# Kernel tuning notes

Hardware: AMD Instinct MI355X
Metric: run time of the kernel (lower is better)

## Reference

```python
import jax, jax.numpy as jnp
import numpy as np

B, C, HC, H, W = 4, 512, 64, 64, 64


def _spectral_norm(Wm, u):
    # one torch-style power iteration; u,v are treated as constants (detached)
    v = Wm.T @ u
    v = v / jnp.maximum(jnp.linalg.norm(v), 1e-12)
    u2 = Wm @ v
    u2 = u2 / jnp.maximum(jnp.linalg.norm(u2), 1e-12)
    u2 = jax.lax.stop_gradient(u2)
    v = jax.lax.stop_gradient(v)
    sigma = u2 @ (Wm @ v)
    return Wm / sigma


def setup_inputs() -> dict:
    key = jax.random.key(0)
    ks = jax.random.split(key, 14)
    return {
        "x": jax.random.normal(ks[0], (B, C, H, W), jnp.float32),
        "Wf": jax.random.normal(ks[1], (HC, C), jnp.float32) * 0.05,
        "bf": jax.random.normal(ks[2], (HC,), jnp.float32) * 0.05,
        "Wg": jax.random.normal(ks[3], (HC, C), jnp.float32) * 0.05,
        "bg": jax.random.normal(ks[4], (HC,), jnp.float32) * 0.05,
        "Wh": jax.random.normal(ks[5], (HC, C), jnp.float32) * 0.05,
        "bh": jax.random.normal(ks[6], (HC,), jnp.float32) * 0.05,
        "Wv": jax.random.normal(ks[7], (C, HC), jnp.float32) * 0.05,
        "bv": jax.random.normal(ks[8], (C,), jnp.float32) * 0.05,
        "uf": jax.random.normal(ks[9], (HC,), jnp.float32),
        "ug": jax.random.normal(ks[10], (HC,), jnp.float32),
        "uh": jax.random.normal(ks[11], (HC,), jnp.float32),
        "uv": jax.random.normal(ks[12], (C,), jnp.float32),
        "gamma": jax.random.normal(ks[13], (1,), jnp.float32),
    }


def reference(x, Wf, bf, Wg, bg, Wh, bh, Wv, bv, uf, ug, uh, uv, gamma):
    nb, nc, imgh, imgw = x.shape
    n = imgh * imgw
    xf = x.reshape(nb, nc, n)  # [B, C, N]
    Wf_sn = _spectral_norm(Wf, uf)
    Wg_sn = _spectral_norm(Wg, ug)
    Wh_sn = _spectral_norm(Wh, uh)
    Wv_sn = _spectral_norm(Wv, uv)
    # 1x1 convs are per-pixel GEMMs
    f = jnp.einsum('kc,bcn->bkn', Wf_sn, xf) + bf[:, None]  # [B, HC, N]
    g = jnp.einsum('kc,bcn->bkn', Wg_sn, xf) + bg[:, None]
    h = jnp.einsum('kc,bcn->bkn', Wh_sn, xf) + bh[:, None]
    s = jnp.einsum('bkn,bkm->bnm', f, g)       # [B, N, N] scores
    beta = jax.nn.softmax(s, axis=-1)
    o = jnp.einsum('bnm,bkm->bkn', beta, h)    # [B, HC, N] (already transposed)
    out = jnp.einsum('ck,bkn->bcn', Wv_sn, o) + bv[:, None]
    out = out.reshape(nb, nc, imgh, imgw)
    return gamma[0] * out + x
```

## Files before the change

kernel.cpp:

```cpp
#include <hip/hip_runtime.h>
#include <hip/hip_bf16.h>

typedef __attribute__((ext_vector_type(8))) short short8;
typedef __attribute__((ext_vector_type(4))) float floatx4;
typedef __attribute__((ext_vector_type(16))) float floatx16;
typedef unsigned short ushortt;

#define LOG2E 1.4426950408889634f

__device__ __forceinline__ float fast_exp2(float x) {
    return __builtin_amdgcn_exp2f(x);
}
__device__ __forceinline__ ushortt f2bf(float f) {
    unsigned int u = __float_as_uint(f);
    u += 0x7fffu + ((u >> 16) & 1u);
    return (ushortt)(u >> 16);
}
__device__ __forceinline__ unsigned int f2bf_pk(float a, float b) {
    float2 t; t.x = a; t.y = b;
    __hip_bfloat162 h = __float22bfloat162_rn(t);
    return *reinterpret_cast<unsigned int*>(&h);
}
__device__ __forceinline__ float bf2f(ushortt h) {
    return __uint_as_float(((unsigned int)h) << 16);
}

__device__ __forceinline__ float block_sum(float v, float* red) {
    #pragma unroll
    for (int off = 32; off > 0; off >>= 1) v += __shfl_down(v, off);
    int wid = threadIdx.x >> 6, ln = threadIdx.x & 63;
    __syncthreads();
    if (ln == 0) red[wid] = v;
    __syncthreads();
    return red[0] + red[1] + red[2] + red[3];
}

__global__ __launch_bounds__(256) void sigma_kernel(
    const float* __restrict__ Wf, const float* __restrict__ uf,
    const float* __restrict__ Wg, const float* __restrict__ ug,
    const float* __restrict__ Wh, const float* __restrict__ uh,
    const float* __restrict__ Wv, const float* __restrict__ uv,
    float* __restrict__ sig,
    ushortt* __restrict__ wqkv, ushortt* __restrict__ wvb) {
    __shared__ float tv[512];
    __shared__ float tvp[256];
    __shared__ float zpart[256];
    __shared__ float red[4];
    __shared__ float ssig;
    const int mat = blockIdx.x, tid = threadIdx.x;

    if (mat < 3) {
        const float* W = (mat == 0) ? Wf : ((mat == 1) ? Wg : Wh);
        const float* u = (mat == 0) ? uf : ((mat == 1) ? ug : uh);
        for (int c = tid; c < 512; c += 256) {
            float s0 = 0.f;
            #pragma unroll 8
            for (int r = 0; r < 64; ++r) s0 += W[r * 512 + c] * u[r];
            tv[c] = s0;
        }
        __syncthreads();
        float p = tv[tid] * tv[tid] + tv[tid + 256] * tv[tid + 256];
        float nt2 = block_sum(p, red);
        float nt = fmaxf(sqrtf(nt2), 1e-12f);
        {
            int r = tid & 63, qq = tid >> 6;
            const float* Wr = W + r * 512 + qq * 128;
            const float* tq = tv + qq * 128;
            float part = 0.f;
            #pragma unroll 16
            for (int c = 0; c < 128; ++c) part += Wr[c] * tq[c];
            zpart[tid] = part;
        }
        __syncthreads();
        if (tid < 64) {
            float z = zpart[tid] + zpart[tid + 64] + zpart[tid + 128] + zpart[tid + 192];
            z = z * z;
            #pragma unroll
            for (int off = 32; off > 0; off >>= 1) z += __shfl_xor(z, off);
            if (tid == 0) {
                float sg0 = sqrtf(z) / nt;
                sig[mat] = sg0;
                ssig = sg0;
            }
        }
        __syncthreads();
        float inv = 1.0f / ssig;
        const float4* W4 = reinterpret_cast<const float4*>(W);
        unsigned int* dst = reinterpret_cast<unsigned int*>(wqkv + mat * 32768);
        for (int i = tid; i < 8192; i += 256) {
            float4 wv = W4[i];
            dst[2 * i]     = f2bf_pk(wv.x * inv, wv.y * inv);
            dst[2 * i + 1] = f2bf_pk(wv.z * inv, wv.w * inv);
        }
    } else {
        const float* W = Wv; const float* u = uv;
        {
            int c = tid & 63, rs = tid >> 6;
            float s0 = 0.f;
            #pragma unroll 8
            for (int r = rs * 128; r < rs * 128 + 128; ++r) s0 += W[r * 64 + c] * u[r];
            tvp[tid] = s0;
        }
        __syncthreads();
        if (tid < 64) tv[tid] = tvp[tid] + tvp[tid + 64] + tvp[tid + 128] + tvp[tid + 192];
        __syncthreads();
        float t = (tid < 64) ? tv[tid] : 0.f;
        float nt2 = block_sum(t * t, red);
        float nt = fmaxf(sqrtf(nt2), 1e-12f);
        float sg3;
        {
            const float* w1 = W + (size_t)tid * 64;
            const float* w2 = W + (size_t)(tid + 256) * 64;
            float z1 = 0.f, z2 = 0.f;
            #pragma unroll 8
            for (int c = 0; c < 64; ++c) {
                float tc = tv[c];
                z1 += w1[c] * tc;
                z2 += w2[c] * tc;
            }
            float zp = z1 * z1 + z2 * z2;
            float z2t = block_sum(zp, red);
            sg3 = sqrtf(z2t) / nt;
            if (tid == 0) sig[3] = sg3;
        }
        float inv = 1.0f / sg3;
        const float4* W4 = reinterpret_cast<const float4*>(W);
        unsigned int* dst = reinterpret_cast<unsigned int*>(wvb);
        for (int i = tid; i < 8192; i += 256) {
            float4 wv = W4[i];
            dst[2 * i]     = f2bf_pk(wv.x * inv, wv.y * inv);
            dst[2 * i + 1] = f2bf_pk(wv.z * inv, wv.w * inv);
        }
    }
}

__global__ __launch_bounds__(256, 4) void qkv_kernel(
    const float* __restrict__ x, const ushortt* __restrict__ wqkv,
    const float* __restrict__ bfv, const float* __restrict__ bgv,
    const float* __restrict__ bhv,
    ushortt* __restrict__ Qb, ushortt* __restrict__ Kb, ushortt* __restrict__ Vt) {
    __shared__ unsigned int xs[2048];
    const int tid = threadIdx.x;
    const int n0 = blockIdx.x * 32, b = blockIdx.y;
    const int lane = tid & 63, w = tid >> 6;
    const int strip = w & 1, ksel = w >> 1;
    const int q = lane >> 4, l15 = lane & 15;
    const int sn = tid & 31, sg = tid >> 5;

    floatx4 acc[6];
    #pragma unroll
    for (int kt = 0; kt < 6; ++kt) acc[kt] = (floatx4){0.f, 0.f, 0.f, 0.f};

    const float* xb = x + ((size_t)b * 512) * 4096 + n0 + sn;
    const int sslot = sn * 32 + ((sg ^ (sn & 7)) << 2);
    float2 pre[4];
    #pragma unroll
    for (int i = 0; i < 4; ++i) {
        int c = sg * 8 + 2 * i;
        pre[i].x = xb[(size_t)c * 4096];
        pre[i].y = xb[(size_t)(c + 1) * 4096];
    }
    {
        uint4 pk;
        pk.x = f2bf_pk(pre[0].x, pre[0].y);
        pk.y = f2bf_pk(pre[1].x, pre[1].y);
        pk.z = f2bf_pk(pre[2].x, pre[2].y);
        pk.w = f2bf_pk(pre[3].x, pre[3].y);
        *reinterpret_cast<uint4*>(&xs[sslot]) = pk;
    }
    #pragma unroll
    for (int i = 0; i < 4; ++i) {
        int c = 64 + sg * 8 + 2 * i;
        pre[i].x = xb[(size_t)c * 4096];
        pre[i].y = xb[(size_t)(c + 1) * 4096];
    }

    for (int it = 0; it < 8; ++it) {
        __syncthreads();
        if (it < 7) {
            uint4 pk;
            pk.x = f2bf_pk(pre[0].x, pre[0].y);
            pk.y = f2bf_pk(pre[1].x, pre[1].y);
            pk.z = f2bf_pk(pre[2].x, pre[2].y);
            pk.w = f2bf_pk(pre[3].x, pre[3].y);
            *reinterpret_cast<uint4*>(&xs[(((it + 1) & 1) << 10) + sslot]) = pk;
        }
        if (it < 6) {
            #pragma unroll
            for (int i = 0; i < 4; ++i) {
                int c = (it + 2) * 64 + sg * 8 + 2 * i;
                pre[i].x = xb[(size_t)c * 4096];
                pre[i].y = xb[(size_t)(c + 1) * 4096];
            }
        }
        const int c0 = it * 64;
        const unsigned int* xr = &xs[((it & 1) << 10) + (16 * strip + l15) * 32];
        #pragma unroll
        for (int kc = 0; kc < 2; ++kc) {
            union { uint4 v; short8 s8; } af;
            af.v = *reinterpret_cast<const uint4*>(&xr[((4 * kc + q) ^ (l15 & 7)) << 2]);
            #pragma unroll
            for (int kt = 0; kt < 6; ++kt) {
                short8 bb = *reinterpret_cast<const short8*>(
                    &wqkv[(size_t)(ksel * 96 + kt * 16 + l15) * 512 + c0 + kc * 32 + q * 8]);
                acc[kt] = __builtin_amdgcn_mfma_f32_16x16x32_bf16(af.s8, bb, acc[kt], 0, 0, 0);
            }
        }
    }

    const int nloc = n0 + 16 * strip + 4 * q;
    if (ksel == 0) {
        #pragma unroll
        for (int kt = 0; kt < 4; ++kt) {
            int k = kt * 16 + l15;
            float bb = bfv[k];
            #pragma unroll
            for (int r = 0; r < 4; ++r)
                Qb[((size_t)b * 4096 + nloc + r) * 64 + k] = f2bf((acc[kt][r] + bb) * LOG2E);
        }
        #pragma unroll
        for (int kt = 4; kt < 6; ++kt) {
            int k = (kt - 4) * 16 + l15;
            float bb = bgv[k];
            #pragma unroll
            for (int r = 0; r < 4; ++r)
                Kb[((size_t)b * 4096 + nloc + r) * 64 + k] = f2bf(acc[kt][r] + bb);
        }
    } else {
        #pragma unroll
        for (int kt = 0; kt < 2; ++kt) {
            int k = 32 + kt * 16 + l15;
            float bb = bgv[k];
            #pragma unroll
            for (int r = 0; r < 4; ++r)
                Kb[((size_t)b * 4096 + nloc + r) * 64 + k] = f2bf(acc[kt][r] + bb);
        }
    }
    __syncthreads();
    if (ksel == 1) {
        #pragma unroll
        for (int kt = 2; kt < 6; ++kt) {
            int d = (kt - 2) * 16 + l15;
            float bb = bhv[d];
            int base = d * 17 + 8 * strip + 2 * q;
            xs[base]     = f2bf_pk(acc[kt][0] + bb, acc[kt][1] + bb);
            xs[base + 1] = f2bf_pk(acc[kt][2] + bb, acc[kt][3] + bb);
        }
    }
    __syncthreads();
    {
        int d = tid >> 2, sgg = tid & 3;
        uint4 vv;
        vv.x = xs[d * 17 + sgg * 4 + 0]; vv.y = xs[d * 17 + sgg * 4 + 1];
        vv.z = xs[d * 17 + sgg * 4 + 2]; vv.w = xs[d * 17 + sgg * 4 + 3];
        *reinterpret_cast<uint4*>(&Vt[((size_t)b * 64 + d) * 4096 + n0 + sgg * 8]) = vv;
    }
}

__global__ __launch_bounds__(256, 3) void attn_kernel(
    const ushortt* __restrict__ Qb, const ushortt* __restrict__ Kb,
    const ushortt* __restrict__ Vt, ushortt* __restrict__ Opart,
    float2* __restrict__ ml, ushortt* __restrict__ Ob, int KB) {
    __shared__ unsigned int smem[8448];
    const int tid = threadIdx.x;
    const int n0 = blockIdx.x * 64, b = blockIdx.y, s = blockIdx.z;
    const int lane = tid & 63, w = tid >> 6;
    const int qh = w & 1, kh = w >> 1;
    const int l31 = lane & 31, h = lane >> 5;

    const ushortt* Kg = Kb + (size_t)b * 4096 * 64;
    const ushortt* Vg = Vt + (size_t)b * 64 * 4096;

    short8 bq[4];
    {
        const ushortt* Qg = Qb + ((size_t)b * 4096 + n0 + 32 * qh + l31) * 64;
        #pragma unroll
        for (int kc = 0; kc < 4; ++kc)
            bq[kc] = *reinterpret_cast<const short8*>(Qg + kc * 16 + 8 * h);
    }

    floatx16 ot0 = {}, ot1 = {};
    float m_i = -1e30f, l_i = 0.f;

    const int row = tid >> 2, seg = tid & 3;
    const int kbeg = s * KB, kend = kbeg + KB;
    const int rsw = row & 7;
    const int ws0 = row * 32 + ((((2 * seg)) ^ rsw) << 2);
    const int ws1 = row * 32 + ((((2 * seg + 1)) ^ rsw) << 2);

    uint4 ck0, ck1, cv0, cv1;
    {
        int nb = kbeg * 64;
        const ushortt* kp = Kg + (size_t)(nb + row) * 64 + seg * 16;
        ck0 = *reinterpret_cast<const uint4*>(kp);
        ck1 = *reinterpret_cast<const uint4*>(kp + 8);
        const ushortt* vp = Vg + (size_t)row * 4096 + nb + seg * 16;
        cv0 = *reinterpret_cast<const uint4*>(vp);
        cv1 = *reinterpret_cast<const uint4*>(vp + 8);
    }
    *reinterpret_cast<uint4*>(&smem[ws0]) = ck0;
    *reinterpret_cast<uint4*>(&smem[ws1]) = ck1;
    *reinterpret_cast<uint4*>(&smem[2048 + ws0]) = cv0;
    *reinterpret_cast<uint4*>(&smem[2048 + ws1]) = cv1;
    if (kbeg + 1 < kend) {
        int nb = (kbeg + 1) * 64;
        const ushortt* kp = Kg + (size_t)(nb + row) * 64 + seg * 16;
        ck0 = *reinterpret_cast<const uint4*>(kp);
        ck1 = *reinterpret_cast<const uint4*>(kp + 8);
        const ushortt* vp = Vg + (size_t)row * 4096 + nb + seg * 16;
        cv0 = *reinterpret_cast<const uint4*>(vp);
        cv1 = *reinterpret_cast<const uint4*>(vp + 8);
    }

    for (int kb = kbeg; kb < kend; ++kb) {
        const int cur = (kb - kbeg) & 1;
        const unsigned int rb = cur ? 4096u : 0u;
        const unsigned int wbs = cur ? 0u : 4096u;
        __syncthreads();
        if (kb + 1 < kend) {
            *reinterpret_cast<uint4*>(&smem[wbs + ws0]) = ck0;
            *reinterpret_cast<uint4*>(&smem[wbs + ws1]) = ck1;
            *reinterpret_cast<uint4*>(&smem[wbs + 2048 + ws0]) = cv0;
            *reinterpret_cast<uint4*>(&smem[wbs + 2048 + ws1]) = cv1;
        }
        if (kb + 2 < kend) {
            int nb = (kb + 2) * 64;
            const ushortt* kp = Kg + (size_t)(nb + row) * 64 + seg * 16;
            ck0 = *reinterpret_cast<const uint4*>(kp);
            ck1 = *reinterpret_cast<const uint4*>(kp + 8);
            const ushortt* vp = Vg + (size_t)row * 4096 + nb + seg * 16;
            cv0 = *reinterpret_cast<const uint4*>(vp);
            cv1 = *reinterpret_cast<const uint4*>(vp + 8);
        }

        floatx16 st = {};
        const unsigned int* kr = &smem[rb + (32 * kh + l31) * 32];
        const int esw = l31 & 7;
        #pragma unroll
        for (int kc = 0; kc < 4; ++kc) {
            union { uint4 v; short8 s8; } af;
            af.v = *reinterpret_cast<const uint4*>(&kr[((2 * kc + h) ^ esw) << 2]);
            st = __builtin_amdgcn_mfma_f32_32x32x16_bf16(af.s8, bq[kc], st, 0, 0, 0);
        }

        float mx = fmaxf(fmaxf(fmaxf(st[0], st[1]), fmaxf(st[2], st[3])),
                         fmaxf(fmaxf(st[4], st[5]), fmaxf(st[6], st[7])));
        float mx2 = fmaxf(fmaxf(fmaxf(st[8], st[9]), fmaxf(st[10], st[11])),
                          fmaxf(fmaxf(st[12], st[13]), fmaxf(st[14], st[15])));
        mx = fmaxf(mx, mx2);
        mx = fmaxf(mx, __shfl_xor(mx, 32));
        if (!__all(mx <= m_i + 8.f)) {
            float mn = fmaxf(m_i, mx);
            float alpha = fast_exp2(m_i - mn);
            m_i = mn;
            l_i *= alpha;
            #pragma unroll
            for (int r = 0; r < 16; ++r) { ot0[r] *= alpha; ot1[r] *= alpha; }
        }
        float p[16], rs = 0.f;
        #pragma unroll
        for (int r = 0; r < 16; ++r) { p[r] = fast_exp2(st[r] - m_i); rs += p[r]; }
        rs += __shfl_xor(rs, 32);
        l_i += rs;

        unsigned int pk[8], sp[8];
        #pragma unroll
        for (int i = 0; i < 8; ++i) pk[i] = f2bf_pk(p[2 * i], p[2 * i + 1]);
        #pragma unroll
        for (int i = 0; i < 8; ++i) sp[i] = (unsigned int)__shfl_xor((int)pk[i], 32);
        union { unsigned int u[4]; short8 s8; } pb0, pb1;
        pb0.u[0] = h ? sp[2] : pk[0]; pb0.u[1] = h ? sp[3] : pk[1];
        pb0.u[2] = h ? pk[2] : sp[0]; pb0.u[3] = h ? pk[3] : sp[1];
        pb1.u[0] = h ? sp[6] : pk[4]; pb1.u[1] = h ? sp[7] : pk[5];
        pb1.u[2] = h ? pk[6] : sp[4]; pb1.u[3] = h ? pk[7] : sp[5];

        const unsigned int* vr0 = &smem[rb + 2048 + l31 * 32];
        const unsigned int* vr1 = &smem[rb + 2048 + (32 + l31) * 32];
        #pragma unroll
        for (int c = 0; c < 2; ++c) {
            union { uint4 v; short8 s8; } af;
            af.v = *reinterpret_cast<const uint4*>(&vr0[((4 * kh + 2 * c + h) ^ esw) << 2]);
            ot0 = __builtin_amdgcn_mfma_f32_32x32x16_bf16(af.s8, c ? pb1.s8 : pb0.s8, ot0, 0, 0, 0);
            af.v = *reinterpret_cast<const uint4*>(&vr1[((4 * kh + 2 * c + h) ^ esw) << 2]);
            ot1 = __builtin_amdgcn_mfma_f32_32x32x16_bf16(af.s8, c ? pb1.s8 : pb0.s8, ot1, 0, 0, 0);
        }
    }

    __syncthreads();
    if (h == 0) {
        smem[8192 + w * 32 + l31] = __float_as_uint(m_i);
        smem[8320 + w * 32 + l31] = __float_as_uint(l_i);
    }
    __syncthreads();
    int pw = 2 * (1 - kh) + qh;
    float m2 = __uint_as_float(smem[8192 + pw * 32 + l31]);
    float l2 = __uint_as_float(smem[8320 + pw * 32 + l31]);
    float mstar = fmaxf(m_i, m2);
    float wself = fast_exp2(m_i - mstar);
    float w2 = fast_exp2(m2 - mstar);
    float lm = wself * l_i + w2 * l2;
    float sc = (gridDim.z == 1) ? (wself / lm) : wself;
    if (gridDim.z > 1 && kh == 0 && h == 0) {
        float2 v; v.x = mstar; v.y = lm;
        ml[((size_t)s * 4 + b) * 4096 + n0 + 32 * qh + l31] = v;
    }
    float* om = reinterpret_cast<float*>(smem);
    if (kh == 0) {
        #pragma unroll
        for (int r = 0; r < 16; ++r) {
            int d0 = (r & 3) + 8 * (r >> 2) + 4 * h;
            om[(32 * qh + l31) * 65 + d0] = sc * ot0[r];
            om[(32 * qh + l31) * 65 + 32 + d0] = sc * ot1[r];
        }
    }
    __syncthreads();
    if (kh == 1) {
        #pragma unroll
        for (int r = 0; r < 16; ++r) {
            int d0 = (r & 3) + 8 * (r >> 2) + 4 * h;
            om[(32 * qh + l31) * 65 + d0] += sc * ot0[r];
            om[(32 * qh + l31) * 65 + 32 + d0] += sc * ot1[r];
        }
    }
    __syncthreads();
    {
        int qq = tid >> 2, dsg = tid & 3;
        unsigned int pkk[8];
        #pragma unroll
        for (int j = 0; j < 8; ++j)
            pkk[j] = f2bf_pk(om[qq * 65 + dsg * 16 + 2 * j], om[qq * 65 + dsg * 16 + 2 * j + 1]);
        ushortt* base = (gridDim.z == 1)
            ? (Ob + ((size_t)b * 4096 + n0) * 64)
            : (Opart + (((size_t)s * 4 + b) * 4096 + n0) * 64);
        uint4* d4 = reinterpret_cast<uint4*>(base + (size_t)qq * 64 + dsg * 16);
        uint4 o0; o0.x = pkk[0]; o0.y = pkk[1]; o0.z = pkk[2]; o0.w = pkk[3];
        uint4 o1; o1.x = pkk[4]; o1.y = pkk[5]; o1.z = pkk[6]; o1.w = pkk[7];
        d4[0] = o0; d4[1] = o1;
    }
}

__global__ __launch_bounds__(256, 2) void proj_kernel(
    const ushortt* __restrict__ Opart, const float2* __restrict__ ml,
    const ushortt* __restrict__ Ob, const ushortt* __restrict__ wvb,
    const float* __restrict__ bv, const float* __restrict__ gamma,
    const float* __restrict__ x, float* __restrict__ out, int S) {
    __shared__ ushortt ol[32 * 72];
    const int tid = threadIdx.x;
    const int n0 = blockIdx.x * 32, b = blockIdx.y;

    {
        int row = tid >> 3, t8 = tid & 7;
        int rg = n0 + row;
        if (S == 1) {
            uint4 v = *reinterpret_cast<const uint4*>(
                Ob + ((size_t)b * 4096 + rg) * 64 + t8 * 8);
            *reinterpret_cast<uint4*>(&ol[row * 72 + t8 * 8]) = v;
        } else {
            float2 mls[4];
            float m = -1e30f;
            #pragma unroll 4
            for (int s = 0; s < 4; ++s) {
                mls[s] = ml[((size_t)s * 4 + b) * 4096 + rg];
                m = fmaxf(m, mls[s].x);
            }
            float wgt[4], denom = 0.f;
            #pragma unroll 4
            for (int s = 0; s < 4; ++s) {
                wgt[s] = fast_exp2(mls[s].x - m);
                denom += wgt[s] * mls[s].y;
            }
            float inv = 1.0f / denom;
            float acc[8];
            #pragma unroll
            for (int j = 0; j < 8; ++j) acc[j] = 0.f;
            #pragma unroll 4
            for (int s = 0; s < 4; ++s) {
                union { uint4 v; ushortt hh[8]; } u;
                u.v = *reinterpret_cast<const uint4*>(
                    Opart + (((size_t)s * 4 + b) * 4096 + rg) * 64 + t8 * 8);
                float ww = wgt[s];
                #pragma unroll
                for (int j = 0; j < 8; ++j) acc[j] += ww * bf2f(u.hh[j]);
            }
            uint4 v;
            v.x = f2bf_pk(acc[0] * inv, acc[1] * inv);
            v.y = f2bf_pk(acc[2] * inv, acc[3] * inv);
            v.z = f2bf_pk(acc[4] * inv, acc[5] * inv);
            v.w = f2bf_pk(acc[6] * inv, acc[7] * inv);
            *reinterpret_cast<uint4*>(&ol[row * 72 + t8 * 8]) = v;
        }
    }
    __syncthreads();

    const int w = tid >> 6, lane = tid & 63, q = lane >> 4, l15 = lane & 15;
    short8 bfr[2][2];
    #pragma unroll
    for (int u = 0; u < 2; ++u)
        #pragma unroll
        for (int kc = 0; kc < 2; ++kc)
            bfr[u][kc] = *reinterpret_cast<const short8*>(
                &ol[(16 * u + l15) * 72 + 32 * kc + q * 8]);

    floatx4 acc[8][2];
    #pragma unroll
    for (int t = 0; t < 8; ++t)
        #pragma unroll
        for (int u = 0; u < 2; ++u) acc[t][u] = (floatx4){0.f, 0.f, 0.f, 0.f};

    const int cw = w * 128;
    #pragma unroll
    for (int t = 0; t < 8; ++t) {
        short8 a0 = *reinterpret_cast<const short8*>(
            &wvb[(size_t)(cw + 16 * t + l15) * 64 + q * 8]);
        short8 a1 = *reinterpret_cast<const short8*>(
            &wvb[(size_t)(cw + 16 * t + l15) * 64 + 32 + q * 8]);
        #pragma unroll
        for (int u = 0; u < 2; ++u) {
            acc[t][u] = __builtin_amdgcn_mfma_f32_16x16x32_bf16(a0, bfr[u][0], acc[t][u], 0, 0, 0);
            acc[t][u] = __builtin_amdgcn_mfma_f32_16x16x32_bf16(a1, bfr[u][1], acc[t][u], 0, 0, 0);
        }
    }

    float gm = gamma[0];
    #pragma unroll
    for (int t = 0; t < 8; ++t) {
        #pragma unroll
        for (int r = 0; r < 4; ++r) {
            int c = cw + 16 * t + 4 * q + r;
            float bb = bv[c];
            #pragma unroll
            for (int u = 0; u < 2; ++u) {
                int n = n0 + 16 * u + l15;
                size_t idx = ((size_t)(b * 512 + c)) * 4096 + n;
                out[idx] = gm * (acc[t][u][r] + bb) + x[idx];
            }
        }
    }
}

extern "C" void kernel_launch(void* const* d_in, const int* in_sizes, int n_in,
                              void* d_out, int out_size, void* d_ws, size_t ws_size,
                              hipStream_t stream) {
    const float* x   = (const float*)d_in[0];
    const float* Wf  = (const float*)d_in[1];
    const float* bf_ = (const float*)d_in[2];
    const float* Wg  = (const float*)d_in[3];
    const float* bg_ = (const float*)d_in[4];
    const float* Wh  = (const float*)d_in[5];
    const float* bh_ = (const float*)d_in[6];
    const float* Wv  = (const float*)d_in[7];
    const float* bv_ = (const float*)d_in[8];
    const float* uf  = (const float*)d_in[9];
    const float* ug  = (const float*)d_in[10];
    const float* uh  = (const float*)d_in[11];
    const float* uv  = (const float*)d_in[12];
    const float* gm  = (const float*)d_in[13];
    float* out = (float*)d_out;

    char* ws = (char*)d_ws;
    float*   sig   = (float*)ws;
    ushortt* wqkv  = (ushortt*)(ws + 256);
    ushortt* wvb   = (ushortt*)(ws + 196864);
    ushortt* Qb    = (ushortt*)(ws + 262400);
    ushortt* Kb    = (ushortt*)(ws + 2359552);
    ushortt* Vt    = (ushortt*)(ws + 4456704);
    ushortt* Ob    = (ushortt*)(ws + 6553856);
    float2*  ml    = (float2*)(ws + 8651008);
    ushortt* Opart = (ushortt*)(ws + 9175296);

    int S = (ws_size >= (size_t)17563904) ? 4 : 1;

    sigma_kernel<<<4, 256, 0, stream>>>(Wf, uf, Wg, ug, Wh, uh, Wv, uv, sig, wqkv, wvb);
    qkv_kernel<<<dim3(128, 4), 256, 0, stream>>>(x, wqkv, bf_, bg_, bh_, Qb, Kb, Vt);
    attn_kernel<<<dim3(64, 4, S), 256, 0, stream>>>(Qb, Kb, Vt, Opart, ml, Ob, 64 / S);
    proj_kernel<<<dim3(128, 4), 256, 0, stream>>>(Opart, ml, Ob, wvb, bv_, gm, x, out, S);
}
```

Measured before the change: 189.4 us.

## Fuse attention and output projection with per-wave key splits and XCD-aware mapping

Merges the attention and projection kernels into one. Each block now handles 32 queries, and each of its four waves processes a disjoint quarter of the keys using private double-buffered LDS tiles with no block barriers inside the loop. The partial softmax results are merged in LDS, then the Wv projection and residual add run in the same block. This removes the Opart/ml workspace round trip, the split-K grid dimension and one kernel launch. It adds XCD-aware block indexing so each batch maps to the same XCDs for L2 reuse, plus s_setprio around the MFMAs. In exchange, occupancy drops to 2 blocks per CU with larger LDS use, and each wave must load its own K/V tiles.

```diff
diff --git a/kernel.cpp b/kernel.cpp
--- a/kernel.cpp
+++ b/kernel.cpp
@@ -20,9 +20,6 @@
     float2 t; t.x = a; t.y = b;
     __hip_bfloat162 h = __float22bfloat162_rn(t);
     return *reinterpret_cast<unsigned int*>(&h);
-}
-__device__ __forceinline__ float bf2f(ushortt h) {
-    return __uint_as_float(((unsigned int)h) << 16);
 }
 
 __device__ __forceinline__ float block_sum(float v, float* red) {
@@ -257,15 +254,18 @@
     }
 }
 
-__global__ __launch_bounds__(256, 3) void attn_kernel(
+__global__ __launch_bounds__(256, 2) void attn_proj_kernel(
     const ushortt* __restrict__ Qb, const ushortt* __restrict__ Kb,
-    const ushortt* __restrict__ Vt, ushortt* __restrict__ Opart,
-    float2* __restrict__ ml, ushortt* __restrict__ Ob, int KB) {
-    __shared__ unsigned int smem[8448];
+    const ushortt* __restrict__ Vt, const ushortt* __restrict__ wvb,
+    const float* __restrict__ bv, const float* __restrict__ gamma,
+    const float* __restrict__ x, float* __restrict__ out) {
+    __shared__ unsigned int smem[16384];
     const int tid = threadIdx.x;
-    const int n0 = blockIdx.x * 64, b = blockIdx.y, s = blockIdx.z;
+    const int fid = blockIdx.x + 128 * blockIdx.y;
+    const int xcd = fid & 7, idx8 = fid >> 3;
+    const int b = xcd >> 1;
+    const int n0 = ((xcd & 1) * 64 + idx8) * 32;
     const int lane = tid & 63, w = tid >> 6;
-    const int qh = w & 1, kh = w >> 1;
     const int l31 = lane & 31, h = lane >> 5;
 
     const ushortt* Kg = Kb + (size_t)b * 4096 * 64;
@@ -273,7 +273,7 @@
 
     short8 bq[4];
     {
-        const ushortt* Qg = Qb + ((size_t)b * 4096 + n0 + 32 * qh + l31) * 64;
+        const ushortt* Qg = Qb + ((size_t)b * 4096 + n0 + l31) * 64;
         #pragma unroll
         for (int kc = 0; kc < 4; ++kc)
             bq[kc] = *reinterpret_cast<const short8*>(Qg + kc * 16 + 8 * h);
@@ -282,66 +282,57 @@
     floatx16 ot0 = {}, ot1 = {};
     float m_i = -1e30f, l_i = 0.f;
 
-    const int row = tid >> 2, seg = tid & 3;
-    const int kbeg = s * KB, kend = kbeg + KB;
-    const int rsw = row & 7;
-    const int ws0 = row * 32 + ((((2 * seg)) ^ rsw) << 2);
-    const int ws1 = row * 32 + ((((2 * seg + 1)) ^ rsw) << 2);
-
-    uint4 ck0, ck1, cv0, cv1;
-    {
-        int nb = kbeg * 64;
-        const ushortt* kp = Kg + (size_t)(nb + row) * 64 + seg * 16;
-        ck0 = *reinterpret_cast<const uint4*>(kp);
-        ck1 = *reinterpret_cast<const uint4*>(kp + 8);
-        const ushortt* vp = Vg + (size_t)row * 4096 + nb + seg * 16;
-        cv0 = *reinterpret_cast<const uint4*>(vp);
-        cv1 = *reinterpret_cast<const uint4*>(vp + 8);
-    }
-    *reinterpret_cast<uint4*>(&smem[ws0]) = ck0;
-    *reinterpret_cast<uint4*>(&smem[ws1]) = ck1;
-    *reinterpret_cast<uint4*>(&smem[2048 + ws0]) = cv0;
-    *reinterpret_cast<uint4*>(&smem[2048 + ws1]) = cv1;
-    if (kbeg + 1 < kend) {
-        int nb = (kbeg + 1) * 64;
-        const ushortt* kp = Kg + (size_t)(nb + row) * 64 + seg * 16;
-        ck0 = *reinterpret_cast<const uint4*>(kp);
-        ck1 = *reinterpret_cast<const uint4*>(kp + 8);
-        const ushortt* vp = Vg + (size_t)row * 4096 + nb + seg * 16;
-        cv0 = *reinterpret_cast<const uint4*>(vp);
-        cv1 = *reinterpret_cast<const uint4*>(vp + 8);
-    }
-
-    for (int kb = kbeg; kb < kend; ++kb) {
-        const int cur = (kb - kbeg) & 1;
-        const unsigned int rb = cur ? 4096u : 0u;
-        const unsigned int wbs = cur ? 0u : 4096u;
-        __syncthreads();
-        if (kb + 1 < kend) {
-            *reinterpret_cast<uint4*>(&smem[wbs + ws0]) = ck0;
-            *reinterpret_cast<uint4*>(&smem[wbs + ws1]) = ck1;
-            *reinterpret_cast<uint4*>(&smem[wbs + 2048 + ws0]) = cv0;
-            *reinterpret_cast<uint4*>(&smem[wbs + 2048 + ws1]) = cv1;
-        }
-        if (kb + 2 < kend) {
-            int nb = (kb + 2) * 64;
-            const ushortt* kp = Kg + (size_t)(nb + row) * 64 + seg * 16;
-            ck0 = *reinterpret_cast<const uint4*>(kp);
-            ck1 = *reinterpret_cast<const uint4*>(kp + 8);
-            const ushortt* vp = Vg + (size_t)row * 4096 + nb + seg * 16;
-            cv0 = *reinterpret_cast<const uint4*>(vp);
-            cv1 = *reinterpret_cast<const uint4*>(vp + 8);
-        }
+    const int krow = lane >> 3, kseg = lane & 7;
+    const int vsub = lane >> 2, vq = lane & 3;
+    const unsigned wb = (unsigned)w << 12;
+
+    uint4 ck[4], cv[4];
+    auto ldkv = [&](int t) {
+        const int pxb = t * 128 + 32 * w;
+        #pragma unroll
+        for (int p = 0; p < 4; ++p)
+            ck[p] = *reinterpret_cast<const uint4*>(
+                Kg + (size_t)(pxb + 8 * p + krow) * 64 + kseg * 8);
+        #pragma unroll
+        for (int p = 0; p < 4; ++p)
+            cv[p] = *reinterpret_cast<const uint4*>(
+                Vg + (size_t)(16 * p + vsub) * 4096 + pxb + vq * 8);
+    };
+    auto stkv = [&](int buf) {
+        const unsigned kb_ = wb + (buf ? 1024u : 0u);
+        const unsigned vb_ = wb + 2048u + (buf ? 1024u : 0u);
+        #pragma unroll
+        for (int p = 0; p < 4; ++p) {
+            int row = 8 * p + krow;
+            *reinterpret_cast<uint4*>(&smem[kb_ + row * 32 + ((kseg ^ (row & 7)) << 2)]) = ck[p];
+        }
+        #pragma unroll
+        for (int p = 0; p < 4; ++p) {
+            int d = 16 * p + vsub;
+            *reinterpret_cast<uint4*>(&smem[vb_ + d * 16 + ((vq ^ (d & 3)) << 2)]) = cv[p];
+        }
+    };
+
+    ldkv(0); stkv(0); ldkv(1);
+
+    for (int t = 0; t < 32; ++t) {
+        const int cur = t & 1;
+        if (t + 1 < 32) stkv(cur ^ 1);
+        if (t + 2 < 32) ldkv(t + 2);
 
         floatx16 st = {};
-        const unsigned int* kr = &smem[rb + (32 * kh + l31) * 32];
+        const unsigned kb_ = wb + (cur ? 1024u : 0u);
+        const unsigned vb_ = wb + 2048u + (cur ? 1024u : 0u);
         const int esw = l31 & 7;
+        const unsigned int* kr = &smem[kb_ + l31 * 32];
+        __builtin_amdgcn_s_setprio(1);
         #pragma unroll
         for (int kc = 0; kc < 4; ++kc) {
             union { uint4 v; short8 s8; } af;
             af.v = *reinterpret_cast<const uint4*>(&kr[((2 * kc + h) ^ esw) << 2]);
             st = __builtin_amdgcn_mfma_f32_32x32x16_bf16(af.s8, bq[kc], st, 0, 0, 0);
         }
+        __builtin_amdgcn_s_setprio(0);
 
         float mx = fmaxf(fmaxf(fmaxf(st[0], st[1]), fmaxf(st[2], st[3])),
                          fmaxf(fmaxf(st[4], st[5]), fmaxf(st[6], st[7])));
@@ -374,165 +365,115 @@
         pb1.u[0] = h ? sp[6] : pk[4]; pb1.u[1] = h ? sp[7] : pk[5];
         pb1.u[2] = h ? pk[6] : sp[4]; pb1.u[3] = h ? pk[7] : sp[5];
 
-        const unsigned int* vr0 = &smem[rb + 2048 + l31 * 32];
-        const unsigned int* vr1 = &smem[rb + 2048 + (32 + l31) * 32];
+        const unsigned int* vr0 = &smem[vb_ + l31 * 16];
+        const unsigned int* vr1 = &smem[vb_ + (32 + l31) * 16];
+        const int esv = l31 & 3;
+        __builtin_amdgcn_s_setprio(1);
         #pragma unroll
         for (int c = 0; c < 2; ++c) {
             union { uint4 v; short8 s8; } af;
-            af.v = *reinterpret_cast<const uint4*>(&vr0[((4 * kh + 2 * c + h) ^ esw) << 2]);
+            af.v = *reinterpret_cast<const uint4*>(&vr0[((2 * c + h) ^ esv) << 2]);
             ot0 = __builtin_amdgcn_mfma_f32_32x32x16_bf16(af.s8, c ? pb1.s8 : pb0.s8, ot0, 0, 0, 0);
-            af.v = *reinterpret_cast<const uint4*>(&vr1[((4 * kh + 2 * c + h) ^ esw) << 2]);
+            af.v = *reinterpret_cast<const uint4*>(&vr1[((2 * c + h) ^ esv) << 2]);
             ot1 = __builtin_amdgcn_mfma_f32_32x32x16_bf16(af.s8, c ? pb1.s8 : pb0.s8, ot1, 0, 0, 0);
         }
+        __builtin_amdgcn_s_setprio(0);
     }
 
     __syncthreads();
     if (h == 0) {
-        smem[8192 + w * 32 + l31] = __float_as_uint(m_i);
-        smem[8320 + w * 32 + l31] = __float_as_uint(l_i);
-    }
-    __syncthreads();
-    int pw = 2 * (1 - kh) + qh;
-    float m2 = __uint_as_float(smem[8192 + pw * 32 + l31]);
-    float l2 = __uint_as_float(smem[8320 + pw * 32 + l31]);
-    float mstar = fmaxf(m_i, m2);
-    float wself = fast_exp2(m_i - mstar);
-    float w2 = fast_exp2(m2 - mstar);
-    float lm = wself * l_i + w2 * l2;
-    float sc = (gridDim.z == 1) ? (wself / lm) : wself;
-    if (gridDim.z > 1 && kh == 0 && h == 0) {
-        float2 v; v.x = mstar; v.y = lm;
-        ml[((size_t)s * 4 + b) * 4096 + n0 + 32 * qh + l31] = v;
-    }
-    float* om = reinterpret_cast<float*>(smem);
-    if (kh == 0) {
-        #pragma unroll
-        for (int r = 0; r < 16; ++r) {
-            int d0 = (r & 3) + 8 * (r >> 2) + 4 * h;
-            om[(32 * qh + l31) * 65 + d0] = sc * ot0[r];
-            om[(32 * qh + l31) * 65 + 32 + d0] = sc * ot1[r];
-        }
-    }
-    __syncthreads();
-    if (kh == 1) {
-        #pragma unroll
-        for (int r = 0; r < 16; ++r) {
-            int d0 = (r & 3) + 8 * (r >> 2) + 4 * h;
-            om[(32 * qh + l31) * 65 + d0] += sc * ot0[r];
-            om[(32 * qh + l31) * 65 + 32 + d0] += sc * ot1[r];
-        }
+        smem[8704 + w * 32 + l31] = __float_as_uint(m_i);
+        smem[8832 + w * 32 + l31] = __float_as_uint(l_i);
     }
     __syncthreads();
     {
-        int qq = tid >> 2, dsg = tid & 3;
-        unsigned int pkk[8];
-        #pragma unroll
-        for (int j = 0; j < 8; ++j)
-            pkk[j] = f2bf_pk(om[qq * 65 + dsg * 16 + 2 * j], om[qq * 65 + dsg * 16 + 2 * j + 1]);
-        ushortt* base = (gridDim.z == 1)
-            ? (Ob + ((size_t)b * 4096 + n0) * 64)
-            : (Opart + (((size_t)s * 4 + b) * 4096 + n0) * 64);
-        uint4* d4 = reinterpret_cast<uint4*>(base + (size_t)qq * 64 + dsg * 16);
-        uint4 o0; o0.x = pkk[0]; o0.y = pkk[1]; o0.z = pkk[2]; o0.w = pkk[3];
-        uint4 o1; o1.x = pkk[4]; o1.y = pkk[5]; o1.z = pkk[6]; o1.w = pkk[7];
-        d4[0] = o0; d4[1] = o1;
-    }
-}
-
-__global__ __launch_bounds__(256, 2) void proj_kernel(
-    const ushortt* __restrict__ Opart, const float2* __restrict__ ml,
-    const ushortt* __restrict__ Ob, const ushortt* __restrict__ wvb,
-    const float* __restrict__ bv, const float* __restrict__ gamma,
-    const float* __restrict__ x, float* __restrict__ out, int S) {
-    __shared__ ushortt ol[32 * 72];
-    const int tid = threadIdx.x;
-    const int n0 = blockIdx.x * 32, b = blockIdx.y;
-
+        float mstar = -1e30f, mw[4], lw[4];
+        #pragma unroll
+        for (int w2 = 0; w2 < 4; ++w2) {
+            mw[w2] = __uint_as_float(smem[8704 + w2 * 32 + l31]);
+            lw[w2] = __uint_as_float(smem[8832 + w2 * 32 + l31]);
+            mstar = fmaxf(mstar, mw[w2]);
+        }
+        float lm = 0.f;
+        #pragma unroll
+        for (int w2 = 0; w2 < 4; ++w2) lm += fast_exp2(mw[w2] - mstar) * lw[w2];
+        float sc = fast_exp2(m_i - mstar) / lm;
+        float* reg = reinterpret_cast<float*>(&smem[w * 2176]);
+        #pragma unroll
+        for (int k = 0; k < 4; ++k) {
+            float4 v0, v1;
+            v0.x = sc * ot0[4 * k];     v0.y = sc * ot0[4 * k + 1];
+            v0.z = sc * ot0[4 * k + 2]; v0.w = sc * ot0[4 * k + 3];
+            v1.x = sc * ot1[4 * k];     v1.y = sc * ot1[4 * k + 1];
+            v1.z = sc * ot1[4 * k + 2]; v1.w = sc * ot1[4 * k + 3];
+            *reinterpret_cast<float4*>(&reg[l31 * 68 + 8 * k + 4 * h]) = v0;
+            *reinterpret_cast<float4*>(&reg[l31 * 68 + 32 + 8 * k + 4 * h]) = v1;
+        }
+    }
+    __syncthreads();
+    ushortt* ol = reinterpret_cast<ushortt*>(&smem[8960]);
     {
-        int row = tid >> 3, t8 = tid & 7;
-        int rg = n0 + row;
-        if (S == 1) {
-            uint4 v = *reinterpret_cast<const uint4*>(
-                Ob + ((size_t)b * 4096 + rg) * 64 + t8 * 8);
-            *reinterpret_cast<uint4*>(&ol[row * 72 + t8 * 8]) = v;
-        } else {
-            float2 mls[4];
-            float m = -1e30f;
-            #pragma unroll 4
-            for (int s = 0; s < 4; ++s) {
-                mls[s] = ml[((size_t)s * 4 + b) * 4096 + rg];
-                m = fmaxf(m, mls[s].x);
+        const int q = tid >> 3, d8 = (tid & 7) * 8;
+        float s[8];
+        #pragma unroll
+        for (int j = 0; j < 8; ++j) s[j] = 0.f;
+        #pragma unroll
+        for (int w2 = 0; w2 < 4; ++w2) {
+            const float* rr = reinterpret_cast<const float*>(&smem[w2 * 2176]) + q * 68 + d8;
+            float4 a = *reinterpret_cast<const float4*>(rr);
+            float4 b2 = *reinterpret_cast<const float4*>(rr + 4);
+            s[0] += a.x; s[1] += a.y; s[2] += a.z; s[3] += a.w;
+            s[4] += b2.x; s[5] += b2.y; s[6] += b2.z; s[7] += b2.w;
+        }
+        unsigned int* od = reinterpret_cast<unsigned int*>(&ol[q * 72 + d8]);
+        od[0] = f2bf_pk(s[0], s[1]); od[1] = f2bf_pk(s[2], s[3]);
+        od[2] = f2bf_pk(s[4], s[5]); od[3] = f2bf_pk(s[6], s[7]);
+    }
+    __syncthreads();
+
+    {
+        const int q4 = lane >> 4, l15 = lane & 15;
+        short8 bfr[2][2];
+        #pragma unroll
+        for (int u = 0; u < 2; ++u)
+            #pragma unroll
+            for (int kc = 0; kc < 2; ++kc)
+                bfr[u][kc] = *reinterpret_cast<const short8*>(
+                    &ol[(16 * u + l15) * 72 + 32 * kc + q4 * 8]);
+
+        floatx4 acc[8][2];
+        #pragma unroll
+        for (int t = 0; t < 8; ++t)
+            #pragma unroll
+            for (int u = 0; u < 2; ++u) acc[t][u] = (floatx4){0.f, 0.f, 0.f, 0.f};
+
+        const int cw = w * 128;
+        #pragma unroll
+        for (int t = 0; t < 8; ++t) {
+            short8 a0 = *reinterpret_cast<const short8*>(
+                &wvb[(size_t)(cw + 16 * t + l15) * 64 + q4 * 8]);
+            short8 a1 = *reinterpret_cast<const short8*>(
+                &wvb[(size_t)(cw + 16 * t + l15) * 64 + 32 + q4 * 8]);
+            #pragma unroll
+            for (int u = 0; u < 2; ++u) {
+                acc[t][u] = __builtin_amdgcn_mfma_f32_16x16x32_bf16(a0, bfr[u][0], acc[t][u], 0, 0, 0);
+                acc[t][u] = __builtin_amdgcn_mfma_f32_16x16x32_bf16(a1, bfr[u][1], acc[t][u], 0, 0, 0);
             }
-            float wgt[4], denom = 0.f;
-            #pragma unroll 4
-            for (int s = 0; s < 4; ++s) {
-                wgt[s] = fast_exp2(mls[s].x - m);
-                denom += wgt[s] * mls[s].y;
-            }
-            float inv = 1.0f / denom;
-            float acc[8];
-            #pragma unroll
-            for (int j = 0; j < 8; ++j) acc[j] = 0.f;
-            #pragma unroll 4
-            for (int s = 0; s < 4; ++s) {
-                union { uint4 v; ushortt hh[8]; } u;
-                u.v = *reinterpret_cast<const uint4*>(
-                    Opart + (((size_t)s * 4 + b) * 4096 + rg) * 64 + t8 * 8);
-                float ww = wgt[s];
+        }
+
+        float gm = gamma[0];
+        #pragma unroll
+        for (int t = 0; t < 8; ++t) {
+            #pragma unroll
+            for (int r = 0; r < 4; ++r) {
+                int c = cw + 16 * t + 4 * q4 + r;
+                float bb = bv[c];
                 #pragma unroll
-                for (int j = 0; j < 8; ++j) acc[j] += ww * bf2f(u.hh[j]);
-            }
-            uint4 v;
-            v.x = f2bf_pk(acc[0] * inv, acc[1] * inv);
-            v.y = f2bf_pk(acc[2] * inv, acc[3] * inv);
-            v.z = f2bf_pk(acc[4] * inv, acc[5] * inv);
-            v.w = f2bf_pk(acc[6] * inv, acc[7] * inv);
-            *reinterpret_cast<uint4*>(&ol[row * 72 + t8 * 8]) = v;
-        }
-    }
-    __syncthreads();
-
-    const int w = tid >> 6, lane = tid & 63, q = lane >> 4, l15 = lane & 15;
-    short8 bfr[2][2];
-    #pragma unroll
-    for (int u = 0; u < 2; ++u)
-        #pragma unroll
-        for (int kc = 0; kc < 2; ++kc)
-            bfr[u][kc] = *reinterpret_cast<const short8*>(
-                &ol[(16 * u + l15) * 72 + 32 * kc + q * 8]);
-
-    floatx4 acc[8][2];
-    #pragma unroll
-    for (int t = 0; t < 8; ++t)
-        #pragma unroll
-        for (int u = 0; u < 2; ++u) acc[t][u] = (floatx4){0.f, 0.f, 0.f, 0.f};
-
-    const int cw = w * 128;
-    #pragma unroll
-    for (int t = 0; t < 8; ++t) {
-        short8 a0 = *reinterpret_cast<const short8*>(
-            &wvb[(size_t)(cw + 16 * t + l15) * 64 + q * 8]);
-        short8 a1 = *reinterpret_cast<const short8*>(
-            &wvb[(size_t)(cw + 16 * t + l15) * 64 + 32 + q * 8]);
-        #pragma unroll
-        for (int u = 0; u < 2; ++u) {
-            acc[t][u] = __builtin_amdgcn_mfma_f32_16x16x32_bf16(a0, bfr[u][0], acc[t][u], 0, 0, 0);
-            acc[t][u] = __builtin_amdgcn_mfma_f32_16x16x32_bf16(a1, bfr[u][1], acc[t][u], 0, 0, 0);
-        }
-    }
-
-    float gm = gamma[0];
-    #pragma unroll
-    for (int t = 0; t < 8; ++t) {
-        #pragma unroll
-        for (int r = 0; r < 4; ++r) {
-            int c = cw + 16 * t + 4 * q + r;
-            float bb = bv[c];
-            #pragma unroll
-            for (int u = 0; u < 2; ++u) {
-                int n = n0 + 16 * u + l15;
-                size_t idx = ((size_t)(b * 512 + c)) * 4096 + n;
-                out[idx] = gm * (acc[t][u][r] + bb) + x[idx];
+                for (int u = 0; u < 2; ++u) {
+                    int n = n0 + 16 * u + l15;
+                    size_t idx = ((size_t)(b * 512 + c)) * 4096 + n;
+                    out[idx] = gm * (acc[t][u][r] + bb) + x[idx];
+                }
             }
         }
     }
@@ -564,14 +505,8 @@
     ushortt* Qb    = (ushortt*)(ws + 262400);
     ushortt* Kb    = (ushortt*)(ws + 2359552);
     ushortt* Vt    = (ushortt*)(ws + 4456704);
-    ushortt* Ob    = (ushortt*)(ws + 6553856);
-    float2*  ml    = (float2*)(ws + 8651008);
-    ushortt* Opart = (ushortt*)(ws + 9175296);
-
-    int S = (ws_size >= (size_t)17563904) ? 4 : 1;
 
     sigma_kernel<<<4, 256, 0, stream>>>(Wf, uf, Wg, ug, Wh, uh, Wv, uv, sig, wqkv, wvb);
     qkv_kernel<<<dim3(128, 4), 256, 0, stream>>>(x, wqkv, bf_, bg_, bh_, Qb, Kb, Vt);
-    attn_kernel<<<dim3(64, 4, S), 256, 0, stream>>>(Qb, Kb, Vt, Opart, ml, Ob, 64 / S);
-    proj_kernel<<<dim3(128, 4), 256, 0, stream>>>(Opart, ml, Ob, wvb, bv_, gm, x, out, S);
-}
+    attn_proj_kernel<<<dim3(128, 4), 256, 0, stream>>>(Qb, Kb, Vt, wvb, bv_, gm, x, out);
+}
```

New measurement: 255.8 us. +35.1%, slower.
